# Kernel optimization log

Measured on AMD Instinct MI355X. Metric: run time of the kernel, lower is better.

Reference implementation:

```python
import jax, jax.numpy as jnp
import numpy as np

H = 1024          # hidden_size
NH = 16           # num_heads
NKV = 16          # num_kv_heads
HD = 64           # head_dim
INTER = 2048      # intermediate_size
E = 8             # num_experts
TOPK = 2
EPS = 1e-6


def setup_inputs() -> dict:
    key = jax.random.key(0)
    ks = jax.random.split(key, 8)
    B, S = 4, 1024
    total_qkv = (NH + 2 * NKV) * HD
    return {
        "hidden_states": jax.random.normal(ks[0], (B, S, H), dtype=jnp.float32),
        "attention_mask": jnp.zeros((1, 1, S, S), dtype=jnp.float32),
        "input_layernorm": jnp.ones((H,), dtype=jnp.float32),
        "post_attention_layernorm": jnp.ones((H,), dtype=jnp.float32),
        "qkv_w": jax.random.normal(ks[1], (H, total_qkv), dtype=jnp.float32) * 0.02,
        "o_w": jax.random.normal(ks[2], (NH * HD, H), dtype=jnp.float32) * 0.02,
        "router_w": jax.random.normal(ks[3], (H, E), dtype=jnp.float32) * 0.02,
        "gate_up_proj": jax.random.normal(ks[4], (E, H, 2 * INTER), dtype=jnp.float32) * 0.02,
        "down_proj": jax.random.normal(ks[5], (E, INTER, H), dtype=jnp.float32) * 0.02,
    }


def _rmsnorm(x, w):
    var = jnp.mean(x * x, axis=-1, keepdims=True)
    return x * jax.lax.rsqrt(var + EPS) * w


def _attention_block(x, attention_mask, input_layernorm, qkv_w, o_w):
    B, S, _ = x.shape
    h = _rmsnorm(x, input_layernorm)
    qkv = h @ qkv_w  # [B,S,(NH+2*NKV)*HD]
    tq, tkv = NH * HD, NKV * HD
    q = qkv[..., :tq].reshape(B, S, NH, HD).transpose(0, 2, 1, 3)
    k = qkv[..., tq:tq + tkv].reshape(B, S, NKV, HD).transpose(0, 2, 1, 3)
    v = qkv[..., tq + tkv:].reshape(B, S, NKV, HD).transpose(0, 2, 1, 3)
    scores = jnp.einsum('bhqd,bhkd->bhqk', q, k) / np.sqrt(HD).astype(np.float32)
    scores = scores + attention_mask
    attn = jax.nn.softmax(scores, axis=-1)
    out = jnp.einsum('bhqk,bhkd->bhqd', attn, v)
    out = out.transpose(0, 2, 1, 3).reshape(B, S, NH * HD)
    return out @ o_w


def _moe_block(x, post_attention_layernorm, router_w, gate_up_proj, down_proj):
    B, S, _ = x.shape
    xf = x.reshape(-1, H)                      # [T,H]
    T = xf.shape[0]
    hf = _rmsnorm(xf, post_attention_layernorm)
    logits = hf @ router_w                     # [T,E]
    probs = jax.nn.softmax(logits, axis=-1)
    w, idx = jax.lax.top_k(probs, TOPK)        # [T,TOPK]
    w = w / jnp.sum(w, axis=-1, keepdims=True)
    # combine weights scattered into dense [T,E] (0 for unrouted experts)
    cw = jnp.zeros((T, E), dtype=hf.dtype).at[jnp.arange(T)[:, None], idx].add(w)
    out = jnp.zeros_like(hf)
    for e in range(E):  # fixed small expert loop, fully vectorized over tokens
        gu = hf @ gate_up_proj[e]              # [T,2*INTER]
        g, u = gu[:, :INTER], gu[:, INTER:]
        act = jax.nn.silu(g) * u
        out = out + cw[:, e:e + 1] * (act @ down_proj[e])
    return out.reshape(B, S, H)


def reference(hidden_states, attention_mask, input_layernorm, post_attention_layernorm,
              qkv_w, o_w, router_w, gate_up_proj, down_proj):
    x = hidden_states
    x = x + _attention_block(x, attention_mask, input_layernorm, qkv_w, o_w)
    x = x + _moe_block(x, post_attention_layernorm, router_w, gate_up_proj, down_proj)
    return x
```

## Files before the change

kernel.cpp:

```cpp
#include <hip/hip_runtime.h>
#include <cstdint>
#include <cmath>

#define T_TOK 4096
#define H_DIM 1024
#define QKV_N 3072
#define S_LEN 1024
#define INTER_DIM 2048
#define MAXROWS 9216

typedef unsigned short u16;
using f32x4 = __attribute__((ext_vector_type(4))) float;
using h16x8 = __attribute__((ext_vector_type(8))) _Float16;
using h16x4 = __attribute__((ext_vector_type(4))) _Float16;
using i32x4 = __attribute__((ext_vector_type(4))) int;
using u16x4 = __attribute__((ext_vector_type(4))) u16;
using u16x8 = __attribute__((ext_vector_type(8))) u16;

__device__ __forceinline__ float bf2f(u16 u){ return __uint_as_float(((uint32_t)u)<<16); }
__device__ __forceinline__ u16 f2bf(float f){
  uint32_t x = __float_as_uint(f);
  uint32_t r = x + 0x7FFFu + ((x>>16)&1u);
  return (u16)(r>>16);
}
__device__ __forceinline__ f32x4 mfma16(h16x8 a, h16x8 b, f32x4 c){
  return __builtin_amdgcn_mfma_f32_16x16x32_f16(a,b,c,0,0,0);
}
__device__ __forceinline__ float rsqrt_acc(float v){
  float r = rsqrtf(v);
  r = r*(1.5f - 0.5f*v*r*r);
  r = r*(1.5f - 0.5f*v*r*r);
  return r;
}
__device__ __forceinline__ float ldin(const void* p, size_t i, int is32){
  return is32 ? ((const float*)p)[i] : bf2f(((const u16*)p)[i]);
}
__device__ __forceinline__ int kslot_sw(int k, int noct){
  return (k&7) | (((k>>3) ^ (noct&3))<<3);
}
__device__ __forceinline__ void gll16(const void* g, void* l){
  __builtin_amdgcn_global_load_lds(
      (const __attribute__((address_space(1))) void*)g,
      (__attribute__((address_space(3))) void*)l, 16, 0, 0);
}

__global__ void k_detect(const uint32_t* __restrict__ x, int* __restrict__ dflag){
  uint32_t u = x[threadIdx.x];
  int e = (u>>23)&0xFF;
  int ok = (e>=103 && e<=150);
  unsigned long long m = __ballot(ok);
  if (threadIdx.x==0) *dflag = (__popcll(m) >= 48) ? 1 : 0;
}

__global__ __launch_bounds__(256) void k_trans2(const void* __restrict__ src,
    _Float16* __restrict__ dst, int R, int C, const int* __restrict__ df){
  const int is32 = *df;
  __shared__ _Float16 t[64][65];
  size_t bo = (size_t)blockIdx.z * R * C;
  int c0 = blockIdx.x<<6, r0 = blockIdx.y<<6;
  int ty = threadIdx.x>>3, tx = threadIdx.x&7;
  #pragma unroll
  for (int rr=0; rr<2; rr++){
    int r = rr*32 + ty;
    size_t gi = bo + (size_t)(r0+r)*C + c0 + tx*8;
    _Float16 v[8];
    if (is32){
      f32x4 a0 = *(const f32x4*)&((const float*)src)[gi];
      f32x4 a1 = *(const f32x4*)&((const float*)src)[gi+4];
      #pragma unroll
      for (int i=0;i<4;i++){ v[i]=(_Float16)a0[i]; v[4+i]=(_Float16)a1[i]; }
    } else {
      u16x8 a = *(const u16x8*)&((const u16*)src)[gi];
      #pragma unroll
      for (int i=0;i<8;i++) v[i]=(_Float16)bf2f(a[i]);
    }
    #pragma unroll
    for (int i=0;i<8;i++) t[r][tx*8+i] = v[i];
  }
  __syncthreads();
  #pragma unroll
  for (int rr=0; rr<2; rr++){
    int n = rr*32 + ty;
    h16x8 v;
    #pragma unroll
    for (int i=0;i<8;i++) v[i] = t[tx*8+i][n];
    *(h16x8*)&dst[bo + (size_t)(c0+n)*R + r0 + tx*8] = v;
  }
}

__global__ __launch_bounds__(256) void k_maskchk(const void* __restrict__ m, int* __restrict__ flag,
                                                 const int* __restrict__ df){
  const int is32 = *df;
  int i = (blockIdx.x*256 + threadIdx.x)*4;
  int nz = 0;
  if (is32){
    f32x4 v = *(const f32x4*)&((const float*)m)[i];
    nz = (v[0]!=0.f)||(v[1]!=0.f)||(v[2]!=0.f)||(v[3]!=0.f);
  } else {
    u16x4 v = *(const u16x4*)&((const u16*)m)[i];
    nz = ((v[0]|v[1]|v[2]|v[3]) & 0x7FFF) != 0;
  }
  if (nz) atomicOr(flag, 1);
}

__global__ __launch_bounds__(256) void k_rms1(const void* __restrict__ x, const void* __restrict__ w,
                                              _Float16* __restrict__ hhi, _Float16* __restrict__ hlo,
                                              const int* __restrict__ df){
  const int is32 = *df;
  int t = blockIdx.x, tid = threadIdx.x;
  size_t base = (size_t)t*H_DIM + tid*4;
  float f[4];
  #pragma unroll
  for (int m=0;m<4;m++) f[m] = ldin(x, base+m, is32);
  float ss = f[0]*f[0] + f[1]*f[1] + f[2]*f[2] + f[3]*f[3];
  #pragma unroll
  for (int off=32; off>0; off>>=1) ss += __shfl_down(ss, off, 64);
  __shared__ float red[4];
  if ((tid & 63) == 0) red[tid>>6] = ss;
  __syncthreads();
  float rstd = rsqrt_acc((red[0]+red[1]+red[2]+red[3]) * (1.0f/H_DIM) + 1e-6f);
  h16x4 oh, ol;
  #pragma unroll
  for (int m=0;m<4;m++){
    float v = f[m]*rstd*ldin(w, tid*4+m, is32);
    _Float16 hh = (_Float16)v;
    oh[m] = hh;
    ol[m] = (_Float16)(v - (float)hh);
  }
  *(h16x4*)&hhi[base] = oh;
  *(h16x4*)&hlo[base] = ol;
}

template<int EPI>
__global__ __launch_bounds__(256) void k_gemm_hl(const _Float16* __restrict__ Ah,
    const _Float16* __restrict__ Al, const _Float16* __restrict__ Bt,
    float* __restrict__ C, _Float16* __restrict__ Chi, _Float16* __restrict__ Clo,
    const void* __restrict__ res, int N, int K, const int* __restrict__ df){
  const int is32 = (EPI==1) ? *df : 0;
  __shared__ __align__(16) _Float16 AhS[128*32];
  __shared__ __align__(16) _Float16 AlS[128*32];
  __shared__ __align__(16) _Float16 Bs[128*32];
  int tid = threadIdx.x, lane = tid&63, wvx = tid>>6;
  int wr = wvx>>1, wc = wvx&1, quad = lane>>4, lrow = lane&15;
  int m0 = blockIdx.y<<7, n0 = blockIdx.x<<7;
  int ar = tid>>2, acg = (tid&3)*8;
  const _Float16* a0h = &Ah[(size_t)(m0+ar)*K + acg];
  const _Float16* a1h = &Ah[(size_t)(m0+64+ar)*K + acg];
  const _Float16* a0l = &Al[(size_t)(m0+ar)*K + acg];
  const _Float16* a1l = &Al[(size_t)(m0+64+ar)*K + acg];
  const _Float16* b0  = &Bt[(size_t)(n0+ar)*K + acg];
  const _Float16* b1  = &Bt[(size_t)(n0+64+ar)*K + acg];
  f32x4 acc[4][4] = {};
  for (int k0=0; k0<K; k0+=32){
    gll16(a0h + k0, &AhS[wvx*512]);
    gll16(a1h + k0, &AhS[2048 + wvx*512]);
    gll16(a0l + k0, &AlS[wvx*512]);
    gll16(a1l + k0, &AlS[2048 + wvx*512]);
    gll16(b0  + k0, &Bs[wvx*512]);
    gll16(b1  + k0, &Bs[2048 + wvx*512]);
    __syncthreads();
    h16x8 ah[4], al[4], bb[4];
    #pragma unroll
    for (int i=0;i<4;i++){
      ah[i] = *(const h16x8*)&AhS[(wr*64 + i*16 + lrow)*32 + quad*8];
      al[i] = *(const h16x8*)&AlS[(wr*64 + i*16 + lrow)*32 + quad*8];
    }
    #pragma unroll
    for (int j=0;j<4;j++) bb[j] = *(const h16x8*)&Bs[(wc*64 + j*16 + lrow)*32 + quad*8];
    #pragma unroll
    for (int i=0;i<4;i++)
      #pragma unroll
      for (int j=0;j<4;j++){
        acc[i][j] = mfma16(ah[i], bb[j], acc[i][j]);
        acc[i][j] = mfma16(al[i], bb[j], acc[i][j]);
      }
    __syncthreads();
  }
  #pragma unroll
  for (int i=0;i<4;i++)
    #pragma unroll
    for (int j=0;j<4;j++){
      int col = n0 + wc*64 + j*16 + lrow;
      #pragma unroll
      for (int r=0;r<4;r++){
        int row = m0 + wr*64 + i*16 + quad*4 + r;
        size_t idx = (size_t)row*N + col;
        float v = acc[i][j][r];
        if (EPI==1){
          v += ldin(res, idx, is32);
          C[idx] = v;
        } else {
          _Float16 hh = (_Float16)v;
          Chi[idx] = hh;
          Clo[idx] = (_Float16)(v - (float)hh);
        }
      }
    }
}

__global__ __launch_bounds__(256) void k_vt(const _Float16* __restrict__ qh,
    const _Float16* __restrict__ ql, _Float16* __restrict__ vth, _Float16* __restrict__ vtl){
  __shared__ _Float16 th[64][72];
  __shared__ _Float16 tl[64][72];
  int bh = blockIdx.y;
  int b = bh>>4, h = bh&15;
  int key0 = blockIdx.x<<6;
  size_t tok0 = (size_t)b*S_LEN;
  int ty = threadIdx.x>>3, tx = threadIdx.x&7;
  #pragma unroll
  for (int rr=0; rr<2; rr++){
    int r = rr*32 + ty;
    size_t gi = (tok0 + key0 + r)*(size_t)QKV_N + 2048 + h*64 + tx*8;
    h16x8 vh_ = *(const h16x8*)&qh[gi];
    h16x8 vl_ = *(const h16x8*)&ql[gi];
    #pragma unroll
    for (int i=0;i<8;i++){ th[r][tx*8+i] = vh_[i]; tl[r][tx*8+i] = vl_[i]; }
  }
  __syncthreads();
  size_t dbase = (size_t)bh*64*1024;
  #pragma unroll
  for (int rr=0; rr<2; rr++){
    int d = rr*32 + ty;
    h16x8 oh, ol;
    #pragma unroll
    for (int i=0;i<8;i++){ oh[i] = th[tx*8+i][d]; ol[i] = tl[tx*8+i][d]; }
    *(h16x8*)&vth[dbase + (size_t)d*1024 + key0 + tx*8] = oh;
    *(h16x8*)&vtl[dbase + (size_t)d*1024 + key0 + tx*8] = ol;
  }
}

__global__ __launch_bounds__(256, 3) void k_attn(const _Float16* __restrict__ qkvh,
    const _Float16* __restrict__ qkvl, const _Float16* __restrict__ vth_g,
    const _Float16* __restrict__ vtl_g, const void* __restrict__ mask,
    const int* __restrict__ mflag, _Float16* __restrict__ ohi, _Float16* __restrict__ olo,
    const int* __restrict__ df){
  const int is32 = *df;
  __shared__ __align__(16) _Float16 pool[16384];
  int qt = blockIdx.x, bh = blockIdx.y;
  int b = bh>>4, h = bh&15;
  int tid = threadIdx.x, lane = tid&63, wvx = tid>>6, quad = lane>>4, lrow = lane&15;
  size_t tok0 = (size_t)b*S_LEN;
  int q0 = qt<<7;
  {
    int r = tid>>2, cg = (tid&3)*8;
    #pragma unroll
    for (int p=0;p<2;p++)
      #pragma unroll
      for (int g=0;g<2;g++){
        size_t src = (tok0 + q0 + g*64 + r)*(size_t)QKV_N + h*64 + p*32 + cg;
        gll16(&qkvh[src], &pool[p*4096 + g*2048 + wvx*512]);
        gll16(&qkvl[src], &pool[8192 + p*4096 + g*2048 + wvx*512]);
      }
  }
  __syncthreads();
  h16x8 qfh[2][2], qfl[2][2];
  #pragma unroll
  for (int p=0;p<2;p++)
    #pragma unroll
    for (int i=0;i<2;i++){
      qfh[p][i] = *(const h16x8*)&pool[(p*128 + wvx*32 + i*16 + lrow)*32 + quad*8];
      qfl[p][i] = *(const h16x8*)&pool[8192 + (p*128 + wvx*32 + i*16 + lrow)*32 + quad*8];
    }
  _Float16* Khi = pool;
  _Float16* Klo = pool + 2048;
  _Float16* Vth = pool + 4096;
  _Float16* Vtl = pool + 6144;
  _Float16* Phi = pool + 8192;
  _Float16* Plo = pool + 12288;
  int useMask = *mflag;
  float mrun[2][4], lrun[2][4];
  f32x4 oacc[2][4] = {};
  #pragma unroll
  for (int i=0;i<2;i++)
    #pragma unroll
    for (int r=0;r<4;r++){ mrun[i][r] = -INFINITY; lrun[i][r] = 0.f; }
  size_t vbase = (size_t)bh*64*1024;
  int kr = (tid>>2)&31, kp = tid>>7, kcg = (tid&3)*8;
  int vd = tid>>2;

  for (int kt=0; kt<32; kt++){
    int key0 = kt*32;
    __syncthreads();
    {
      size_t ks = (tok0 + key0 + kr)*(size_t)QKV_N + 1024 + h*64 + kp*32 + kcg;
      gll16(&qkvh[ks], &Khi[wvx*512]);
      gll16(&qkvl[ks], &Klo[wvx*512]);
      size_t vs = vbase + (size_t)vd*1024 + key0 + (tid&3)*8;
      gll16(&vth_g[vs], &Vth[wvx*512]);
      gll16(&vtl_g[vs], &Vtl[wvx*512]);
    }
    __syncthreads();
    f32x4 sacc[2][2] = {};
    __builtin_amdgcn_s_setprio(1);
    #pragma unroll
    for (int p=0;p<2;p++){
      h16x8 kh[2], kl[2];
      #pragma unroll
      for (int j=0;j<2;j++){
        kh[j] = *(const h16x8*)&Khi[(p*32 + j*16 + lrow)*32 + quad*8];
        kl[j] = *(const h16x8*)&Klo[(p*32 + j*16 + lrow)*32 + quad*8];
      }
      #pragma unroll
      for (int i=0;i<2;i++)
        #pragma unroll
        for (int j=0;j<2;j++){
          sacc[i][j] = mfma16(qfh[p][i], kh[j], sacc[i][j]);
          sacc[i][j] = mfma16(qfh[p][i], kl[j], sacc[i][j]);
          sacc[i][j] = mfma16(qfl[p][i], kh[j], sacc[i][j]);
        }
    }
    __builtin_amdgcn_s_setprio(0);
    #pragma unroll
    for (int i=0;i<2;i++){
      #pragma unroll
      for (int r=0;r<4;r++){
        int qrow = q0 + wvx*32 + i*16 + quad*4 + r;
        #pragma unroll
        for (int j=0;j<2;j++){
          float s = sacc[i][j][r] * 0.125f;
          if (useMask) s += ldin(mask, (size_t)qrow*S_LEN + key0 + j*16 + lrow, is32);
          sacc[i][j][r] = s;
        }
        float mx = fmaxf(sacc[i][0][r], sacc[i][1][r]);
        #pragma unroll
        for (int mm=1; mm<=8; mm<<=1) mx = fmaxf(mx, __shfl_xor(mx, mm, 64));
        float mnew = fmaxf(mrun[i][r], mx);
        float alpha = __expf(mrun[i][r] - mnew);
        float ps = 0.f;
        #pragma unroll
        for (int j=0;j<2;j++){
          float p = __expf(sacc[i][j][r] - mnew);
          sacc[i][j][r] = p;
          ps += p;
        }
        #pragma unroll
        for (int mm=1; mm<=8; mm<<=1) ps += __shfl_xor(ps, mm, 64);
        lrun[i][r] = lrun[i][r]*alpha + ps;
        mrun[i][r] = mnew;
        #pragma unroll
        for (int j=0;j<4;j++) oacc[i][j][r] *= alpha;
        int prow = wvx*32 + i*16 + quad*4 + r;
        #pragma unroll
        for (int j=0;j<2;j++){
          int key = j*16 + lrow;
          float pv = sacc[i][j][r];
          _Float16 ph = (_Float16)pv;
          Phi[prow*32 + key] = ph;
          Plo[prow*32 + key] = (_Float16)(pv - (float)ph);
        }
      }
    }
    __syncthreads();
    {
      h16x8 pf[2], pl[2], vh[4], vl[4];
      #pragma unroll
      for (int i=0;i<2;i++){
        pf[i] = *(const h16x8*)&Phi[(wvx*32 + i*16 + lrow)*32 + quad*8];
        pl[i] = *(const h16x8*)&Plo[(wvx*32 + i*16 + lrow)*32 + quad*8];
      }
      #pragma unroll
      for (int j=0;j<4;j++){
        vh[j] = *(const h16x8*)&Vth[(j*16 + lrow)*32 + quad*8];
        vl[j] = *(const h16x8*)&Vtl[(j*16 + lrow)*32 + quad*8];
      }
      __builtin_amdgcn_s_setprio(1);
      #pragma unroll
      for (int i=0;i<2;i++)
        #pragma unroll
        for (int j=0;j<4;j++){
          oacc[i][j] = mfma16(pf[i], vh[j], oacc[i][j]);
          oacc[i][j] = mfma16(pf[i], vl[j], oacc[i][j]);
          oacc[i][j] = mfma16(pl[i], vh[j], oacc[i][j]);
        }
      __builtin_amdgcn_s_setprio(0);
    }
  }
  #pragma unroll
  for (int i=0;i<2;i++)
    #pragma unroll
    for (int j=0;j<4;j++)
      #pragma unroll
      for (int r=0;r<4;r++){
        int row = q0 + wvx*32 + i*16 + quad*4 + r;
        int col = h*64 + j*16 + lrow;
        size_t idx = (tok0 + row)*H_DIM + col;
        float v = oacc[i][j][r] / lrun[i][r];
        _Float16 hh = (_Float16)v;
        ohi[idx] = hh;
        olo[idx] = (_Float16)(v - (float)hh);
      }
}

__global__ __launch_bounds__(256) void k_rms2_router(const float* __restrict__ x1, const void* __restrict__ w,
    const void* __restrict__ rw, _Float16* __restrict__ h2,
    int* __restrict__ tok_e, float* __restrict__ tok_w, int* __restrict__ counts,
    const int* __restrict__ df){
  const int is32 = *df;
  int t = blockIdx.x, tid = threadIdx.x;
  f32x4 v = *(const f32x4*)&x1[(size_t)t*H_DIM + tid*4];
  float ss = v[0]*v[0]+v[1]*v[1]+v[2]*v[2]+v[3]*v[3];
  #pragma unroll
  for (int off=32; off>0; off>>=1) ss += __shfl_down(ss, off, 64);
  __shared__ float red[4];
  __shared__ float lgs[32];
  if ((tid&63)==0) red[tid>>6] = ss;
  __syncthreads();
  float rstd = rsqrt_acc((red[0]+red[1]+red[2]+red[3])*(1.0f/H_DIM) + 1e-6f);
  float hv[4];
  h16x4 hst;
  #pragma unroll
  for (int m=0;m<4;m++){ hv[m] = v[m]*rstd*ldin(w, tid*4+m, is32); hst[m] = (_Float16)hv[m]; }
  *(h16x4*)&h2[(size_t)t*H_DIM + tid*4] = hst;
  float part[8] = {0,0,0,0,0,0,0,0};
  #pragma unroll
  for (int m=0;m<4;m++){
    size_t c = (size_t)(tid*4 + m)*8;
    #pragma unroll
    for (int e=0;e<8;e++) part[e] += hv[m]*ldin(rw, c+e, is32);
  }
  #pragma unroll
  for (int e=0;e<8;e++){
    #pragma unroll
    for (int off=32; off>0; off>>=1) part[e] += __shfl_down(part[e], off, 64);
  }
  if ((tid&63)==0){
    #pragma unroll
    for (int e=0;e<8;e++) lgs[(tid>>6)*8 + e] = part[e];
  }
  __syncthreads();
  if (tid==0){
    float lg[8];
    #pragma unroll
    for (int e=0;e<8;e++) lg[e] = lgs[e] + lgs[8+e] + lgs[16+e] + lgs[24+e];
    int e0 = 0;
    #pragma unroll
    for (int e=1;e<8;e++) if (lg[e] > lg[e0]) e0 = e;
    int e1 = (e0==0) ? 1 : 0;
    #pragma unroll
    for (int e=0;e<8;e++) if (e != e0 && lg[e] > lg[e1]) e1 = e;
    float d = expf(lg[e1] - lg[e0]);
    float w0 = 1.0f/(1.0f + d);
    float w1 = d * w0;
    tok_e[t*2] = e0; tok_e[t*2+1] = e1;
    tok_w[t*2] = w0; tok_w[t*2+1] = w1;
    atomicAdd(&counts[e0], 1);
    atomicAdd(&counts[e1], 1);
  }
}

__global__ void k_offsets(const int* __restrict__ counts, int* __restrict__ offs, int* __restrict__ fillpos){
  if (threadIdx.x == 0 && blockIdx.x == 0){
    int o = 0;
    for (int e=0;e<8;e++){
      offs[e] = o; fillpos[e] = o;
      o += (counts[e] + 127) & ~127;
    }
    offs[8] = o;
  }
}

__global__ __launch_bounds__(256) void k_fill(const int* __restrict__ tok_e, const float* __restrict__ tok_w,
    int* __restrict__ fillpos, int* __restrict__ list_ts, float* __restrict__ list_w){
  int t = blockIdx.x*256 + threadIdx.x;
  if (t >= T_TOK) return;
  #pragma unroll
  for (int s=0;s<2;s++){
    int e = tok_e[t*2+s];
    int p = atomicAdd(&fillpos[e], 1);
    list_ts[p] = t*2 + s;
    list_w[p] = tok_w[t*2+s];
  }
}


__global__ __launch_bounds__(256) void k_gemm_gu_t(const _Float16* __restrict__ h2,
    const _Float16* __restrict__ gwt, _Float16* __restrict__ act, const int* __restrict__ list_ts,
    const int* __restrict__ counts, const int* __restrict__ offs){
  int m0 = blockIdx.y<<7;
  if (m0 >= offs[8]) return;
  int e = 0;
  while (m0 >= offs[e+1]) e++;
  int base = offs[e], cnt = counts[e];
  if (m0 >= base + cnt) return;
  __shared__ __align__(16) _Float16 As[128*32], Bg[64*32], Bu[64*32];
  __shared__ int rowtok[128];
  int tid = threadIdx.x;
  if (tid < 128) rowtok[tid] = list_ts[min(m0 + tid, base + cnt - 1)] >> 1;
  __syncthreads();
  int lane = tid&63, wvx = tid>>6, wr = wvx>>1, wc = wvx&1, quad = lane>>4, lrow = lane&15;
  int n0 = blockIdx.x<<6;
  const _Float16* Bge = gwt + (size_t)e*4096*1024 + (size_t)n0*1024;
  const _Float16* Bue = gwt + (size_t)e*4096*1024 + (size_t)(2048+n0)*1024;
  const _Float16* arow0 = &h2[(size_t)rowtok[tid>>2]*H_DIM + (tid&3)*8];
  const _Float16* arow1 = &h2[(size_t)rowtok[(256+tid)>>2]*H_DIM + (tid&3)*8];
  int bR = tid>>2, bG = tid&3;
  f32x4 ag[4][2] = {}, au[4][2] = {};
  for (int k0=0; k0<1024; k0+=32){
    gll16(arow0 + k0, &As[(size_t)(wvx*64)*8]);
    gll16(arow1 + k0, &As[(size_t)(256 + wvx*64)*8]);
    gll16(&Bge[(size_t)bR*1024 + k0 + bG*8], &Bg[(size_t)(wvx*64)*8]);
    gll16(&Bue[(size_t)bR*1024 + k0 + bG*8], &Bu[(size_t)(wvx*64)*8]);
    __syncthreads();
    h16x8 a[4], bg[2], bu[2];
    #pragma unroll
    for (int i=0;i<4;i++) a[i] = *(const h16x8*)&As[(wr*64 + i*16 + lrow)*32 + quad*8];
    #pragma unroll
    for (int j=0;j<2;j++){
      bg[j] = *(const h16x8*)&Bg[(wc*32 + j*16 + lrow)*32 + quad*8];
      bu[j] = *(const h16x8*)&Bu[(wc*32 + j*16 + lrow)*32 + quad*8];
    }
    #pragma unroll
    for (int i=0;i<4;i++)
      #pragma unroll
      for (int j=0;j<2;j++){
        ag[i][j] = mfma16(a[i], bg[j], ag[i][j]);
        au[i][j] = mfma16(a[i], bu[j], au[i][j]);
      }
    __syncthreads();
  }
  #pragma unroll
  for (int i=0;i<4;i++)
    #pragma unroll
    for (int j=0;j<2;j++)
      #pragma unroll
      for (int r=0;r<4;r++){
        int row = m0 + wr*64 + i*16 + quad*4 + r;
        int col = n0 + wc*32 + j*16 + lrow;
        float g = ag[i][j][r], u = au[i][j][r];
        float sv = g / (1.0f + __expf(-g));
        act[(size_t)row*INTER_DIM + col] = (_Float16)(sv * u);
      }
}

__global__ __launch_bounds__(256) void k_gemm_down_t(const _Float16* __restrict__ act,
    const _Float16* __restrict__ dwt, _Float16* __restrict__ slotbuf, const int* __restrict__ list_ts,
    const float* __restrict__ list_w, const int* __restrict__ counts, const int* __restrict__ offs){
  int m0 = blockIdx.y<<7;
  if (m0 >= offs[8]) return;
  int e = 0;
  while (m0 >= offs[e+1]) e++;
  int base = offs[e], cnt = counts[e];
  if (m0 >= base + cnt) return;
  __shared__ __align__(16) _Float16 As[128*32], Bs[128*32];
  int tid = threadIdx.x, lane = tid&63, wvx = tid>>6;
  int wr = wvx>>1, wc = wvx&1, quad = lane>>4, lrow = lane&15;
  int n0 = blockIdx.x<<7;
  const _Float16* Be = dwt + (size_t)e*1024*2048 + (size_t)n0*2048;
  f32x4 acc[4][4] = {};
  for (int k0=0; k0<2048; k0+=32){
    #pragma unroll
    for (int it=0; it<2; it++){
      int c2 = it*256 + tid;
      int r = c2>>2, g = c2&3;
      gll16(&act[(size_t)(m0+r)*INTER_DIM + k0 + g*8], &As[(size_t)(it*256 + wvx*64)*8]);
      gll16(&Be[(size_t)r*2048 + k0 + g*8], &Bs[(size_t)(it*256 + wvx*64)*8]);
    }
    __syncthreads();
    h16x8 a[4], b[4];
    #pragma unroll
    for (int i=0;i<4;i++) a[i] = *(const h16x8*)&As[(wr*64 + i*16 + lrow)*32 + quad*8];
    #pragma unroll
    for (int j=0;j<4;j++) b[j] = *(const h16x8*)&Bs[(wc*64 + j*16 + lrow)*32 + quad*8];
    #pragma unroll
    for (int i=0;i<4;i++)
      #pragma unroll
      for (int j=0;j<4;j++)
        acc[i][j] = mfma16(a[i], b[j], acc[i][j]);
    __syncthreads();
  }
  #pragma unroll
  for (int i=0;i<4;i++)
    #pragma unroll
    for (int r=0;r<4;r++){
      int m = m0 + wr*64 + i*16 + quad*4 + r;
      if (m < base + cnt){
        int ts = list_ts[m];
        float wgt = list_w[m];
        #pragma unroll
        for (int j=0;j<4;j++){
          int col = n0 + wc*64 + j*16 + lrow;
          slotbuf[(size_t)ts*H_DIM + col] = (_Float16)(wgt * acc[i][j][r]);
        }
      }
    }
}


__global__ __launch_bounds__(256) void k_gemm_gu(const _Float16* __restrict__ h2, const void* __restrict__ guw,
    _Float16* __restrict__ act, const int* __restrict__ list_ts,
    const int* __restrict__ counts, const int* __restrict__ offs, const int* __restrict__ df){
  const int is32 = *df;
  int m0 = blockIdx.y<<7;
  if (m0 >= offs[8]) return;
  int e = 0;
  while (m0 >= offs[e+1]) e++;
  int base = offs[e], cnt = counts[e];
  if (m0 >= base + cnt) return;
  __shared__ __align__(16) _Float16 As[128*32], Bg[64*40], Bu[64*40];
  __shared__ int rowtok[128];
  int tid = threadIdx.x;
  if (tid < 128){
    int mc = min(m0 + tid, base + cnt - 1);
    rowtok[tid] = list_ts[mc] >> 1;
  }
  __syncthreads();
  int lane = tid&63, wvx = tid>>6, wr = wvx>>1, wc = wvx&1, quad = lane>>4, lrow = lane&15;
  int n0 = blockIdx.x<<6;
  size_t ebase = (size_t)e*H_DIM*4096;
  f32x4 ag[4][2] = {}, au[4][2] = {};
  for (int k0=0; k0<1024; k0+=32){
    #pragma unroll
    for (int it=0; it<2; it++){
      int ch = it*256 + tid;
      int r = ch>>2, c = ch&3;
      *(i32x4*)&As[ch*8] = *(const i32x4*)&h2[(size_t)rowtok[r]*H_DIM + k0 + c*8];
    }
    {
      int k = tid>>3, g = tid&7;
      size_t rowb = ebase + (size_t)(k0+k)*4096;
      int ks = kslot_sw(k, g);
      _Float16 tg[8], tu[8];
      if (is32){
        const float* gf = (const float*)guw;
        f32x4 a0 = *(const f32x4*)&gf[rowb + n0 + g*8];
        f32x4 a1 = *(const f32x4*)&gf[rowb + n0 + g*8 + 4];
        f32x4 b0 = *(const f32x4*)&gf[rowb + 2048 + n0 + g*8];
        f32x4 b1 = *(const f32x4*)&gf[rowb + 2048 + n0 + g*8 + 4];
        #pragma unroll
        for (int i=0;i<4;i++){ tg[i]=(_Float16)a0[i]; tg[4+i]=(_Float16)a1[i];
                               tu[i]=(_Float16)b0[i]; tu[4+i]=(_Float16)b1[i]; }
      } else {
        const u16* gb = (const u16*)guw;
        u16x4 a0 = *(const u16x4*)&gb[rowb + n0 + g*8];
        u16x4 a1 = *(const u16x4*)&gb[rowb + n0 + g*8 + 4];
        u16x4 b0 = *(const u16x4*)&gb[rowb + 2048 + n0 + g*8];
        u16x4 b1 = *(const u16x4*)&gb[rowb + 2048 + n0 + g*8 + 4];
        #pragma unroll
        for (int i=0;i<4;i++){ tg[i]=(_Float16)bf2f(a0[i]); tg[4+i]=(_Float16)bf2f(a1[i]);
                               tu[i]=(_Float16)bf2f(b0[i]); tu[4+i]=(_Float16)bf2f(b1[i]); }
      }
      #pragma unroll
      for (int i=0;i<8;i++){
        int n = g*8 + i;
        Bg[n*40 + ks] = tg[i];
        Bu[n*40 + ks] = tu[i];
      }
    }
    __syncthreads();
    h16x8 a[4], bg[2], bu[2];
    #pragma unroll
    for (int i=0;i<4;i++) a[i] = *(const h16x8*)&As[(wr*64 + i*16 + lrow)*32 + quad*8];
    #pragma unroll
    for (int j=0;j<2;j++){
      int n = wc*32 + j*16 + lrow;
      int oct = (quad ^ ((n>>3)&3))*8;
      bg[j] = *(const h16x8*)&Bg[n*40 + oct];
      bu[j] = *(const h16x8*)&Bu[n*40 + oct];
    }
    #pragma unroll
    for (int i=0;i<4;i++)
      #pragma unroll
      for (int j=0;j<2;j++){
        ag[i][j] = mfma16(a[i], bg[j], ag[i][j]);
        au[i][j] = mfma16(a[i], bu[j], au[i][j]);
      }
    __syncthreads();
  }
  #pragma unroll
  for (int i=0;i<4;i++)
    #pragma unroll
    for (int j=0;j<2;j++)
      #pragma unroll
      for (int r=0;r<4;r++){
        int row = m0 + wr*64 + i*16 + quad*4 + r;
        int col = n0 + wc*32 + j*16 + lrow;
        float g = ag[i][j][r], u = au[i][j][r];
        float sv = g / (1.0f + __expf(-g));
        act[(size_t)row*INTER_DIM + col] = (_Float16)(sv * u);
      }
}

__global__ __launch_bounds__(256) void k_gemm_down(const _Float16* __restrict__ act, const void* __restrict__ dw,
    _Float16* __restrict__ slotbuf, const int* __restrict__ list_ts, const float* __restrict__ list_w,
    const int* __restrict__ counts, const int* __restrict__ offs, const int* __restrict__ df){
  const int is32 = *df;
  int m0 = blockIdx.y<<7;
  if (m0 >= offs[8]) return;
  int e = 0;
  while (m0 >= offs[e+1]) e++;
  int base = offs[e], cnt = counts[e];
  if (m0 >= base + cnt) return;
  __shared__ __align__(16) _Float16 As[128*32], Bs[128*40];
  int tid = threadIdx.x, lane = tid&63, wvx = tid>>6;
  int wr = wvx>>1, wc = wvx&1, quad = lane>>4, lrow = lane&15;
  int n0 = blockIdx.x<<7;
  size_t ebase = (size_t)e*INTER_DIM*H_DIM;
  f32x4 acc[4][4] = {};
  for (int k0=0; k0<2048; k0+=32){
    #pragma unroll
    for (int it=0; it<2; it++){
      int ch = it*256 + tid;
      int r = ch>>2, c = ch&3;
      *(i32x4*)&As[ch*8] = *(const i32x4*)&act[(size_t)(m0+r)*INTER_DIM + k0 + c*8];
    }
    {
      int k = tid>>3, g = tid&7;
      size_t rowb = ebase + (size_t)(k0+k)*H_DIM;
      int ks = kslot_sw(k, g);
      #pragma unroll
      for (int p=0;p<2;p++){
        _Float16 tb[8];
        if (is32){
          const float* bf = (const float*)dw;
          f32x4 a0 = *(const f32x4*)&bf[rowb + n0 + p*64 + g*8];
          f32x4 a1 = *(const f32x4*)&bf[rowb + n0 + p*64 + g*8 + 4];
          #pragma unroll
          for (int i=0;i<4;i++){ tb[i]=(_Float16)a0[i]; tb[4+i]=(_Float16)a1[i]; }
        } else {
          const u16* bb = (const u16*)dw;
          u16x4 a0 = *(const u16x4*)&bb[rowb + n0 + p*64 + g*8];
          u16x4 a1 = *(const u16x4*)&bb[rowb + n0 + p*64 + g*8 + 4];
          #pragma unroll
          for (int i=0;i<4;i++){ tb[i]=(_Float16)bf2f(a0[i]); tb[4+i]=(_Float16)bf2f(a1[i]); }
        }
        #pragma unroll
        for (int i=0;i<8;i++){
          int n = p*64 + g*8 + i;
          Bs[n*40 + ks] = tb[i];
        }
      }
    }
    __syncthreads();
    h16x8 a[4], b[4];
    #pragma unroll
    for (int i=0;i<4;i++) a[i] = *(const h16x8*)&As[(wr*64 + i*16 + lrow)*32 + quad*8];
    #pragma unroll
    for (int j=0;j<4;j++){
      int n = wc*64 + j*16 + lrow;
      b[j] = *(const h16x8*)&Bs[n*40 + ((quad ^ ((n>>3)&3))*8)];
    }
    #pragma unroll
    for (int i=0;i<4;i++)
      #pragma unroll
      for (int j=0;j<4;j++)
        acc[i][j] = mfma16(a[i], b[j], acc[i][j]);
    __syncthreads();
  }
  #pragma unroll
  for (int i=0;i<4;i++)
    #pragma unroll
    for (int r=0;r<4;r++){
      int m = m0 + wr*64 + i*16 + quad*4 + r;
      if (m < base + cnt){
        int ts = list_ts[m];
        float wgt = list_w[m];
        #pragma unroll
        for (int j=0;j<4;j++){
          int col = n0 + wc*64 + j*16 + lrow;
          slotbuf[(size_t)ts*H_DIM + col] = (_Float16)(wgt * acc[i][j][r]);
        }
      }
    }
}

__global__ __launch_bounds__(256) void k_final(const float* __restrict__ x1, const _Float16* __restrict__ slot,
                                               void* __restrict__ outv, const int* __restrict__ df){
  const int is32 = *df;
  int i4 = (blockIdx.x*256 + threadIdx.x)*4;
  int t = i4 >> 10, c = i4 & 1023;
  f32x4 a = *(const f32x4*)&x1[i4];
  h16x4 s0 = *(const h16x4*)&slot[(size_t)(t*2)*H_DIM + c];
  h16x4 s1 = *(const h16x4*)&slot[(size_t)(t*2+1)*H_DIM + c];
  if (is32){
    f32x4 o;
    #pragma unroll
    for (int m=0;m<4;m++) o[m] = a[m] + (float)s0[m] + (float)s1[m];
    *(f32x4*)&((float*)outv)[i4] = o;
  } else {
    u16x4 o;
    #pragma unroll
    for (int m=0;m<4;m++) o[m] = f2bf(a[m] + (float)s0[m] + (float)s1[m]);
    *(u16x4*)&((u16*)outv)[i4] = o;
  }
}

extern "C" void kernel_launch(void* const* d_in, const int* in_sizes, int n_in,
                              void* d_out, int out_size, void* d_ws, size_t ws_size,
                              hipStream_t stream){
  (void)in_sizes; (void)n_in; (void)out_size;
  const void* x    = d_in[0];
  const void* mask = d_in[1];
  const void* ln1  = d_in[2];
  const void* ln2  = d_in[3];
  const void* qkvw = d_in[4];
  const void* ow   = d_in[5];
  const void* rw   = d_in[6];
  const void* guw  = d_in[7];
  const void* dww  = d_in[8];

  char* ws = (char*)d_ws;
  size_t off = 0;
  auto alloc = [&](size_t b)->void*{ void* p = ws + off; off = (off + b + 255) & ~(size_t)255; return p; };
  int* meta            = (int*)alloc(32*sizeof(int));
  _Float16* qkv_wt     = (_Float16*)alloc((size_t)3072*1024*2);
  _Float16* o_wt       = (_Float16*)alloc((size_t)1024*1024*2);
  _Float16* hpair      = (_Float16*)alloc((size_t)2*4096*1024*2);
  _Float16* qkvpair    = (_Float16*)alloc((size_t)2*4096*3072*2);
  float* x1            = (float*)alloc((size_t)4096*1024*4);
  int* list_ts         = (int*)alloc(MAXROWS*4);
  float* list_w        = (float*)alloc(MAXROWS*4);
  int* tok_e           = (int*)alloc((size_t)4096*2*4);
  float* tok_w         = (float*)alloc((size_t)4096*2*4);
  size_t base_end = off;
  _Float16* gu_wt      = (_Float16*)alloc((size_t)8*4096*1024*2);
  _Float16* down_wt    = (_Float16*)alloc((size_t)8*1024*2048*2);
  const int big = (ws_size >= off) ? 1 : 0;
  (void)base_end;

  int* counts = meta;
  int* offs   = meta + 8;
  int* fillpos= meta + 17;
  int* flag   = meta + 25;
  int* dflag  = meta + 26;

  _Float16* h_hi   = hpair;
  _Float16* h_lo   = hpair + (size_t)4096*1024;
  _Float16* qkv_hi = qkvpair;
  _Float16* qkv_lo = qkvpair + (size_t)4096*3072;
  _Float16* vth    = (_Float16*)x1;
  _Float16* vtl    = vth + (size_t)64*64*1024;
  _Float16* ahi    = hpair;
  _Float16* alo    = hpair + (size_t)4096*1024;
  _Float16* h2     = qkvpair;
  _Float16* act    = qkvpair + (size_t)4096*1024;
  _Float16* slotbuf= hpair;

  hipMemsetAsync(meta, 0, 32*sizeof(int), stream);
  k_detect<<<dim3(1), dim3(64), 0, stream>>>((const uint32_t*)x, dflag);
  k_trans2<<<dim3(48, 16, 1), 256, 0, stream>>>(qkvw, qkv_wt, 1024, 3072, dflag);
  k_trans2<<<dim3(16, 16, 1), 256, 0, stream>>>(ow, o_wt, 1024, 1024, dflag);
  if (big){
    k_trans2<<<dim3(64, 16, 8), 256, 0, stream>>>(guw, gu_wt, 1024, 4096, dflag);
    k_trans2<<<dim3(16, 32, 8), 256, 0, stream>>>(dww, down_wt, 2048, 1024, dflag);
  }
  k_maskchk<<<dim3(1024), 256, 0, stream>>>(mask, flag, dflag);
  k_rms1<<<dim3(4096), 256, 0, stream>>>(x, ln1, h_hi, h_lo, dflag);
  k_gemm_hl<0><<<dim3(24, 32), 256, 0, stream>>>(h_hi, h_lo, qkv_wt, nullptr, qkv_hi, qkv_lo,
                                                 nullptr, 3072, 1024, dflag);
  k_vt<<<dim3(16, 64), 256, 0, stream>>>(qkv_hi, qkv_lo, vth, vtl);
  k_attn<<<dim3(8, 64), 256, 0, stream>>>(qkv_hi, qkv_lo, vth, vtl, mask, flag, ahi, alo, dflag);
  k_gemm_hl<1><<<dim3(8, 32), 256, 0, stream>>>(ahi, alo, o_wt, x1, nullptr, nullptr,
                                                x, 1024, 1024, dflag);
  k_rms2_router<<<dim3(4096), 256, 0, stream>>>(x1, ln2, rw, h2, tok_e, tok_w, counts, dflag);
  k_offsets<<<dim3(1), dim3(64), 0, stream>>>(counts, offs, fillpos);
  k_fill<<<dim3(16), 256, 0, stream>>>(tok_e, tok_w, fillpos, list_ts, list_w);
  if (big){
    k_gemm_gu_t<<<dim3(32, 72), 256, 0, stream>>>(h2, gu_wt, act, list_ts, counts, offs);
    k_gemm_down_t<<<dim3(8, 72), 256, 0, stream>>>(act, down_wt, slotbuf, list_ts, list_w, counts, offs);
  } else {
    k_gemm_gu<<<dim3(32, 72), 256, 0, stream>>>(h2, guw, act, list_ts, counts, offs, dflag);
    k_gemm_down<<<dim3(8, 72), 256, 0, stream>>>(act, dww, slotbuf, list_ts, list_w, counts, offs, dflag);
  }
  k_final<<<dim3(4096), 256, 0, stream>>>(x1, slotbuf, d_out, dflag);
}
```

Measured before the change: 884.2 us.

## Double key tile to 64, register-prefetch K/V, swizzle LDS in attention

The flash-attention kernel now processes 64 keys per iteration instead of 32, halving the loop trip count and the number of barriers. K/V tiles for the next iteration are prefetched into registers while the current tile computes, replacing the synchronous global-to-LDS loads. LDS layouts for K, V and P use an XOR swizzle to reduce bank conflicts. In exchange, LDS doubles to 64KB and register pressure rises, so the occupancy hint drops from 3 to 2 blocks per CU.

```diff
diff --git a/kernel.cpp b/kernel.cpp
--- a/kernel.cpp
+++ b/kernel.cpp
@@ -229,13 +229,19 @@
   }
 }
 
-__global__ __launch_bounds__(256, 3) void k_attn(const _Float16* __restrict__ qkvh,
+__global__ __launch_bounds__(256, 2) void k_attn(const _Float16* __restrict__ qkvh,
     const _Float16* __restrict__ qkvl, const _Float16* __restrict__ vth_g,
     const _Float16* __restrict__ vtl_g, const void* __restrict__ mask,
     const int* __restrict__ mflag, _Float16* __restrict__ ohi, _Float16* __restrict__ olo,
     const int* __restrict__ df){
   const int is32 = *df;
-  __shared__ __align__(16) _Float16 pool[16384];
+  __shared__ __align__(16) _Float16 pool[32768];
+  _Float16* Khi = pool;
+  _Float16* Klo = pool + 4096;
+  _Float16* Vth = pool + 8192;
+  _Float16* Vtl = pool + 12288;
+  _Float16* Phi = pool + 16384;
+  _Float16* Plo = pool + 24576;
   int qt = blockIdx.x, bh = blockIdx.y;
   int b = bh>>4, h = bh&15;
   int tid = threadIdx.x, lane = tid&63, wvx = tid>>6, quad = lane>>4, lrow = lane&15;
@@ -261,12 +267,6 @@
       qfh[p][i] = *(const h16x8*)&pool[(p*128 + wvx*32 + i*16 + lrow)*32 + quad*8];
       qfl[p][i] = *(const h16x8*)&pool[8192 + (p*128 + wvx*32 + i*16 + lrow)*32 + quad*8];
     }
-  _Float16* Khi = pool;
-  _Float16* Klo = pool + 2048;
-  _Float16* Vth = pool + 4096;
-  _Float16* Vtl = pool + 6144;
-  _Float16* Phi = pool + 8192;
-  _Float16* Plo = pool + 12288;
   int useMask = *mflag;
   float mrun[2][4], lrun[2][4];
   f32x4 oacc[2][4] = {};
@@ -275,35 +275,56 @@
     #pragma unroll
     for (int r=0;r<4;r++){ mrun[i][r] = -INFINITY; lrun[i][r] = 0.f; }
   size_t vbase = (size_t)bh*64*1024;
-  int kr = (tid>>2)&31, kp = tid>>7, kcg = (tid&3)*8;
-  int vd = tid>>2;
-
-  for (int kt=0; kt<32; kt++){
-    int key0 = kt*32;
-    __syncthreads();
+  int krow = tid>>3;
+  int c8   = (tid&7)*8;
+  int rsw  = ((tid>>3)&7)<<3;
+  int fsw  = (lrow&7)<<3;
+  size_t ksrc0 = (tok0 + krow)*(size_t)QKV_N + 1024 + h*64 + c8;
+  size_t vsrc0 = vbase + (size_t)krow*1024 + c8;
+  h16x8 kh_r[2], kl_r[2], vh_r[2], vl_r[2];
+  {
+    size_t ks0 = ksrc0, ks1 = ksrc0 + (size_t)32*QKV_N;
+    kh_r[0] = *(const h16x8*)&qkvh[ks0];  kl_r[0] = *(const h16x8*)&qkvl[ks0];
+    kh_r[1] = *(const h16x8*)&qkvh[ks1];  kl_r[1] = *(const h16x8*)&qkvl[ks1];
+    size_t vs0 = vsrc0, vs1 = vsrc0 + 32*1024;
+    vh_r[0] = *(const h16x8*)&vth_g[vs0]; vl_r[0] = *(const h16x8*)&vtl_g[vs0];
+    vh_r[1] = *(const h16x8*)&vth_g[vs1]; vl_r[1] = *(const h16x8*)&vtl_g[vs1];
+  }
+  __syncthreads();
+
+  for (int kt=0; kt<16; kt++){
+    int key0 = kt*64;
     {
-      size_t ks = (tok0 + key0 + kr)*(size_t)QKV_N + 1024 + h*64 + kp*32 + kcg;
-      gll16(&qkvh[ks], &Khi[wvx*512]);
-      gll16(&qkvl[ks], &Klo[wvx*512]);
-      size_t vs = vbase + (size_t)vd*1024 + key0 + (tid&3)*8;
-      gll16(&vth_g[vs], &Vth[wvx*512]);
-      gll16(&vtl_g[vs], &Vtl[wvx*512]);
-    }
-    __syncthreads();
-    f32x4 sacc[2][2] = {};
+      int o0 = (tid*8) ^ rsw, o1 = (2048 + tid*8) ^ rsw;
+      *(h16x8*)&Khi[o0] = kh_r[0];  *(h16x8*)&Khi[o1] = kh_r[1];
+      *(h16x8*)&Klo[o0] = kl_r[0];  *(h16x8*)&Klo[o1] = kl_r[1];
+      *(h16x8*)&Vth[o0] = vh_r[0];  *(h16x8*)&Vth[o1] = vh_r[1];
+      *(h16x8*)&Vtl[o0] = vl_r[0];  *(h16x8*)&Vtl[o1] = vl_r[1];
+    }
+    if (kt < 15){
+      size_t ks0 = ksrc0 + (size_t)(key0+64)*QKV_N, ks1 = ks0 + (size_t)32*QKV_N;
+      kh_r[0] = *(const h16x8*)&qkvh[ks0];  kl_r[0] = *(const h16x8*)&qkvl[ks0];
+      kh_r[1] = *(const h16x8*)&qkvh[ks1];  kl_r[1] = *(const h16x8*)&qkvl[ks1];
+      size_t vs0 = vsrc0 + (key0+64), vs1 = vs0 + 32*1024;
+      vh_r[0] = *(const h16x8*)&vth_g[vs0]; vl_r[0] = *(const h16x8*)&vtl_g[vs0];
+      vh_r[1] = *(const h16x8*)&vth_g[vs1]; vl_r[1] = *(const h16x8*)&vtl_g[vs1];
+    }
+    __syncthreads();
+    f32x4 sacc[2][4] = {};
     __builtin_amdgcn_s_setprio(1);
     #pragma unroll
     for (int p=0;p<2;p++){
-      h16x8 kh[2], kl[2];
-      #pragma unroll
-      for (int j=0;j<2;j++){
-        kh[j] = *(const h16x8*)&Khi[(p*32 + j*16 + lrow)*32 + quad*8];
-        kl[j] = *(const h16x8*)&Klo[(p*32 + j*16 + lrow)*32 + quad*8];
+      h16x8 kh[4], kl[4];
+      #pragma unroll
+      for (int j=0;j<4;j++){
+        int kidx = ((j*16+lrow)*64 + p*32 + quad*8) ^ fsw;
+        kh[j] = *(const h16x8*)&Khi[kidx];
+        kl[j] = *(const h16x8*)&Klo[kidx];
       }
       #pragma unroll
       for (int i=0;i<2;i++)
         #pragma unroll
-        for (int j=0;j<2;j++){
+        for (int j=0;j<4;j++){
           sacc[i][j] = mfma16(qfh[p][i], kh[j], sacc[i][j]);
           sacc[i][j] = mfma16(qfh[p][i], kl[j], sacc[i][j]);
           sacc[i][j] = mfma16(qfl[p][i], kh[j], sacc[i][j]);
@@ -315,22 +336,23 @@
       #pragma unroll
       for (int r=0;r<4;r++){
         int qrow = q0 + wvx*32 + i*16 + quad*4 + r;
-        #pragma unroll
-        for (int j=0;j<2;j++){
-          float s = sacc[i][j][r] * 0.125f;
-          if (useMask) s += ldin(mask, (size_t)qrow*S_LEN + key0 + j*16 + lrow, is32);
-          sacc[i][j][r] = s;
-        }
-        float mx = fmaxf(sacc[i][0][r], sacc[i][1][r]);
+        float s[4];
+        #pragma unroll
+        for (int j=0;j<4;j++){
+          float sv = sacc[i][j][r] * 0.125f;
+          if (useMask) sv += ldin(mask, (size_t)qrow*S_LEN + key0 + j*16 + lrow, is32);
+          s[j] = sv;
+        }
+        float mx = fmaxf(fmaxf(s[0],s[1]), fmaxf(s[2],s[3]));
         #pragma unroll
         for (int mm=1; mm<=8; mm<<=1) mx = fmaxf(mx, __shfl_xor(mx, mm, 64));
         float mnew = fmaxf(mrun[i][r], mx);
         float alpha = __expf(mrun[i][r] - mnew);
         float ps = 0.f;
         #pragma unroll
-        for (int j=0;j<2;j++){
-          float p = __expf(sacc[i][j][r] - mnew);
-          sacc[i][j][r] = p;
+        for (int j=0;j<4;j++){
+          float p = __expf(s[j] - mnew);
+          s[j] = p;
           ps += p;
         }
         #pragma unroll
@@ -338,42 +360,52 @@
         lrun[i][r] = lrun[i][r]*alpha + ps;
         mrun[i][r] = mnew;
         #pragma unroll
-        for (int j=0;j<4;j++) oacc[i][j][r] *= alpha;
+        for (int jd=0;jd<4;jd++) oacc[i][jd][r] *= alpha;
         int prow = wvx*32 + i*16 + quad*4 + r;
-        #pragma unroll
-        for (int j=0;j<2;j++){
-          int key = j*16 + lrow;
-          float pv = sacc[i][j][r];
+        int pswz = (prow&7)<<3;
+        #pragma unroll
+        for (int j=0;j<4;j++){
+          int pidx = (prow*64 + j*16 + lrow) ^ pswz;
+          float pv = s[j];
           _Float16 ph = (_Float16)pv;
-          Phi[prow*32 + key] = ph;
-          Plo[prow*32 + key] = (_Float16)(pv - (float)ph);
+          Phi[pidx] = ph;
+          Plo[pidx] = (_Float16)(pv - (float)ph);
         }
       }
     }
     __syncthreads();
     {
-      h16x8 pf[2], pl[2], vh[4], vl[4];
-      #pragma unroll
-      for (int i=0;i<2;i++){
-        pf[i] = *(const h16x8*)&Phi[(wvx*32 + i*16 + lrow)*32 + quad*8];
-        pl[i] = *(const h16x8*)&Plo[(wvx*32 + i*16 + lrow)*32 + quad*8];
-      }
-      #pragma unroll
-      for (int j=0;j<4;j++){
-        vh[j] = *(const h16x8*)&Vth[(j*16 + lrow)*32 + quad*8];
-        vl[j] = *(const h16x8*)&Vtl[(j*16 + lrow)*32 + quad*8];
-      }
+      h16x8 pf[2][2], pl[2][2];
+      #pragma unroll
+      for (int i=0;i<2;i++)
+        #pragma unroll
+        for (int ks=0;ks<2;ks++){
+          int pidx = ((wvx*32 + i*16 + lrow)*64 + ks*32 + quad*8) ^ fsw;
+          pf[i][ks] = *(const h16x8*)&Phi[pidx];
+          pl[i][ks] = *(const h16x8*)&Plo[pidx];
+        }
       __builtin_amdgcn_s_setprio(1);
       #pragma unroll
-      for (int i=0;i<2;i++)
-        #pragma unroll
-        for (int j=0;j<4;j++){
-          oacc[i][j] = mfma16(pf[i], vh[j], oacc[i][j]);
-          oacc[i][j] = mfma16(pf[i], vl[j], oacc[i][j]);
-          oacc[i][j] = mfma16(pl[i], vh[j], oacc[i][j]);
-        }
+      for (int ks=0;ks<2;ks++){
+        h16x8 vh[4], vl[4];
+        #pragma unroll
+        for (int jd=0;jd<4;jd++){
+          int vidx = ((jd*16+lrow)*64 + ks*32 + quad*8) ^ fsw;
+          vh[jd] = *(const h16x8*)&Vth[vidx];
+          vl[jd] = *(const h16x8*)&Vtl[vidx];
+        }
+        #pragma unroll
+        for (int i=0;i<2;i++)
+          #pragma unroll
+          for (int jd=0;jd<4;jd++){
+            oacc[i][jd] = mfma16(pf[i][ks], vh[jd], oacc[i][jd]);
+            oacc[i][jd] = mfma16(pf[i][ks], vl[jd], oacc[i][jd]);
+            oacc[i][jd] = mfma16(pl[i][ks], vh[jd], oacc[i][jd]);
+          }
+      }
       __builtin_amdgcn_s_setprio(0);
     }
+    __syncthreads();
   }
   #pragma unroll
   for (int i=0;i<2;i++)
```

Measured after the change: 849.3 us. 1.04x faster.
